# Kernel optimization log

Hardware: AMD Instinct MI355X
Metric: run time of the kernel (lower is better)

## Reference

```python
import jax, jax.numpy as jnp
import numpy as np

WS = 14            # window side (14x14 patches)
DIM = 768          # model dim (ViT-Base)
H = 12             # heads
HD = DIM // H      # head dim = 64
B = 128            # batch
N = WS * WS + 1    # 197 tokens (patches + CLS)
NRD = (2 * WS - 1) ** 2 + 3  # num_relative_distance = 732


def _rel_index():
    # Faithful replication of the torch buffer construction.
    coords = np.stack(np.meshgrid(np.arange(WS), np.arange(WS), indexing='ij'))  # [2,WS,WS]
    flat = coords.reshape(2, -1)                                   # [2, WS*WS]
    rel = flat[:, :, None] - flat[:, None, :]                      # [2, P, P]
    rel = rel.transpose(1, 2, 0).astype(np.int64)                  # [P, P, 2]
    rel[:, :, 0] += WS - 1
    rel[:, :, 1] += WS - 1
    rel[:, :, 0] *= 2 * WS - 1
    idx = np.zeros((N, N), dtype=np.int64)
    idx[1:, 1:] = rel.sum(-1)
    idx[0, :] = NRD - 3
    idx[:, 0] = NRD - 2
    idx[0, 0] = NRD - 1
    return jnp.asarray(idx, dtype=jnp.int32)


def setup_inputs() -> dict:
    key = jax.random.key(0)
    ks = jax.random.split(key, 5)
    return {
        'x': jax.random.normal(ks[0], (B, N, DIM), dtype=jnp.float32),
        'qkv_w': jax.random.normal(ks[1], (3 * DIM, DIM), dtype=jnp.float32) * 0.02,
        'q_bias': jnp.zeros((DIM,), jnp.float32),
        'v_bias': jnp.zeros((DIM,), jnp.float32),
        'rpb_table': jax.random.normal(ks[2], (NRD, H), dtype=jnp.float32) * 0.02,
        'proj_w': jax.random.normal(ks[3], (DIM, DIM), dtype=jnp.float32) * 0.02,
        'proj_b': jnp.zeros((DIM,), jnp.float32),
        'rel_idx': _rel_index(),
    }


def reference(x, qkv_w, q_bias, v_bias, rpb_table, proj_w, proj_b, rel_idx):
    Bv, Nv, C = x.shape
    scale = HD ** -0.5
    # qkv_bias = cat(q_bias, zeros, v_bias); eval mode so dropout is identity
    bias = jnp.concatenate([q_bias, jnp.zeros_like(v_bias), v_bias])
    qkv = x @ qkv_w.T + bias                                   # [B,N,3*DIM]
    qkv = qkv.reshape(Bv, Nv, 3, H, HD).transpose(2, 0, 3, 1, 4)
    q, k, v = qkv[0] * scale, qkv[1], qkv[2]                   # [B,H,N,HD]
    attn = jnp.einsum('bhqd,bhkd->bhqk', q, k)                 # [B,H,N,N]
    rpb = rpb_table[rel_idx]                                   # gather -> [N,N,H]
    attn = attn + rpb.transpose(2, 0, 1)[None]                 # + [1,H,N,N]
    attn = jax.nn.softmax(attn, axis=-1)
    out = jnp.einsum('bhqk,bhkd->bhqd', attn, v)               # [B,H,N,HD]
    out = out.transpose(0, 2, 1, 3).reshape(Bv, Nv, H * HD)
    return out @ proj_w.T + proj_b
```

## Files before the change

kernel.cpp:

```cpp
#include <hip/hip_runtime.h>
#include <hip/hip_bf16.h>
#include <cstdint>

#define BATCH 128
#define NTOK  197
#define NHEAD 12

typedef __attribute__((ext_vector_type(8))) __bf16 bf16x8;
typedef __attribute__((ext_vector_type(4))) float f32x4;
typedef __attribute__((ext_vector_type(4))) unsigned short ushort4v;

#define KSTR 72

__device__ __forceinline__ unsigned short f2bf(float f) {
    union { float f; unsigned int u; } v; v.f = f;
    unsigned int r = (v.u + 0x7FFFu + ((v.u >> 16) & 1u)) >> 16;
    return (unsigned short)r;
}

__device__ __forceinline__ void async_cp16(const void* gsrc, void* lds_dst) {
    __builtin_amdgcn_global_load_lds(
        (const __attribute__((address_space(1))) unsigned int*)((uintptr_t)gsrc),
        (__attribute__((address_space(3))) unsigned int*)((uintptr_t)lds_dst),
        16, 0, 0);
}

__global__ void bias_tiles(const float* __restrict__ rpb,
                           const int* __restrict__ rel_idx,
                           float* __restrict__ BT) {
    int idx = blockIdx.x * 256 + threadIdx.x;
    int r    = idx & 3;
    int j    = (idx >> 2) & 3;
    int l16  = (idx >> 4) & 15;
    int quad = (idx >> 8) & 3;
    int kt   = (idx >> 10) & 3;
    int qt   = (idx >> 12) & 15;
    int h    = idx >> 16;
    int qn = qt * 16 + quad * 4 + r; if (qn > 196) qn = 196;
    int kn = kt * 64 + j * 16 + l16;
    float v = 0.f;
    if (kn < NTOK) v = rpb[rel_idx[qn * NTOK + kn] * NHEAD + h];
    BT[idx] = v;
}

__global__ __launch_bounds__(256) void cvt_bf16(const float4* __restrict__ src,
                                                ushort4v* __restrict__ dst, int n4) {
    int i = blockIdx.x * 256 + threadIdx.x;
    if (i >= n4) return;
    float4 f = src[i];
    ushort4v o;
    o.x = f2bf(f.x); o.y = f2bf(f.y); o.z = f2bf(f.z); o.w = f2bf(f.w);
    dst[i] = o;
}

template <int EPI>
__global__ __launch_bounds__(256) void gemm_mfma(
    const unsigned short* __restrict__ A,
    const unsigned short* __restrict__ W,
    const float* __restrict__ bias1, const float* __restrict__ bias2,
    unsigned short* __restrict__ oq, unsigned short* __restrict__ ok,
    unsigned short* __restrict__ ov, float* __restrict__ outf,
    int Mc) {
    __shared__ unsigned short As[128 * 32];
    __shared__ unsigned short Bs[128 * 32];

    const int t    = threadIdx.x;
    const int lane = t & 63;
    const int wave = t >> 6;
    const int wm   = wave >> 1;
    const int wn   = wave & 1;
    const int quad = lane >> 4;
    const int l16  = lane & 15;
    const int m0   = blockIdx.y * 128;
    const int n0   = blockIdx.x * 128;

    const int srow = lane >> 2;
    const int scol = (lane & 3) * 8;
    int ar0 = m0 + wave * 32 + srow;      if (ar0 >= Mc) ar0 = Mc - 1;
    int ar1 = m0 + wave * 32 + 16 + srow; if (ar1 >= Mc) ar1 = Mc - 1;
    const unsigned short* Ag0 = A + (size_t)ar0 * 768 + scol;
    const unsigned short* Ag1 = A + (size_t)ar1 * 768 + scol;
    const unsigned short* Wg0 = W + (size_t)(n0 + wave * 32 + srow) * 768 + scol;
    const unsigned short* Wg1 = Wg0 + (size_t)16 * 768;
    unsigned short* Ad0 = As + (wave * 32) * 32;
    unsigned short* Ad1 = As + (wave * 32 + 16) * 32;
    unsigned short* Bd0 = Bs + (wave * 32) * 32;
    unsigned short* Bd1 = Bs + (wave * 32 + 16) * 32;

    const unsigned short* Afp = As + (wm * 64 + l16) * 32 + quad * 8;
    const unsigned short* Bfp = Bs + (wn * 64 + l16) * 32 + quad * 8;

    f32x4 acc[4][4] = {};

    for (int k0 = 0; k0 < 768; k0 += 32) {
        __syncthreads();
        async_cp16(Ag0 + k0, Ad0);
        async_cp16(Ag1 + k0, Ad1);
        async_cp16(Wg0 + k0, Bd0);
        async_cp16(Wg1 + k0, Bd1);
        __syncthreads();
        bf16x8 af[4], bfr[4];
#pragma unroll
        for (int i = 0; i < 4; i++) af[i]  = *(const bf16x8*)(Afp + i * 16 * 32);
#pragma unroll
        for (int j = 0; j < 4; j++) bfr[j] = *(const bf16x8*)(Bfp + j * 16 * 32);
#pragma unroll
        for (int i = 0; i < 4; i++)
#pragma unroll
            for (int j = 0; j < 4; j++)
                acc[i][j] = __builtin_amdgcn_mfma_f32_16x16x32_bf16(
                    af[i], bfr[j], acc[i][j], 0, 0, 0);
    }

    if (EPI == 0) {
        const int part   = n0 / 768;
        const float scale = (part == 0) ? 0.125f : 1.f;
        unsigned short* dst = (part == 0) ? oq : (part == 1 ? ok : ov);
        const int nb0 = n0 - part * 768;
#pragma unroll
        for (int j = 0; j < 4; j++) {
            const int nnb = nb0 + wn * 64 + j * 16;
            const int h   = nnb >> 6;
            const int d   = (nnb & 63) + l16;
            const float bb = (part == 0) ? bias1[nnb + l16]
                           : (part == 2 ? bias2[nnb + l16] : 0.f);
#pragma unroll
            for (int i = 0; i < 4; i++) {
                const int mb = m0 + wm * 64 + i * 16 + quad * 4;
#pragma unroll
                for (int r = 0; r < 4; r++) {
                    const int m = mb + r;
                    if (m < Mc) {
                        const int bi  = m / NTOK;
                        const int tok = m - bi * NTOK;
                        dst[(((size_t)bi * NHEAD + h) * NTOK + tok) * 64 + d] =
                            f2bf((acc[i][j][r] + bb) * scale);
                    }
                }
            }
        }
    } else {
#pragma unroll
        for (int j = 0; j < 4; j++) {
            const int col = n0 + wn * 64 + j * 16 + l16;
            const float bb = bias1[col];
#pragma unroll
            for (int i = 0; i < 4; i++) {
                const int mb = m0 + wm * 64 + i * 16 + quad * 4;
#pragma unroll
                for (int r = 0; r < 4; r++) {
                    const int m = mb + r;
                    if (m < Mc) outf[(size_t)m * 768 + col] = acc[i][j][r] + bb;
                }
            }
        }
    }
}

__global__ __launch_bounds__(256, 2) void attn_mfma(
    const unsigned short* __restrict__ Q, const unsigned short* __restrict__ K,
    const unsigned short* __restrict__ V, const float* __restrict__ BT,
    unsigned short* __restrict__ AO) {
    __shared__ unsigned short Ks[64 * KSTR];
    __shared__ unsigned short Vt[64 * KSTR];
    __shared__ unsigned short Ps[4][64 * KSTR];

    const int t    = threadIdx.x;
    const int lane = t & 63;
    const int wave = t >> 6;
    const int quad = lane >> 4;
    const int l16  = lane & 15;
    const int bh   = blockIdx.x;
    const int b    = bh / NHEAD;
    const int h    = bh - b * NHEAD;

    const unsigned short* qb = Q + (size_t)bh * NTOK * 64;
    const unsigned short* kb = K + (size_t)bh * NTOK * 64;
    const unsigned short* vb = V + (size_t)bh * NTOK * 64;

    bf16x8 qf[4][2];
#pragma unroll
    for (int i = 0; i < 4; i++) {
        int tok = wave * 64 + i * 16 + l16; if (tok > 196) tok = 196;
#pragma unroll
        for (int ks = 0; ks < 2; ks++)
            qf[i][ks] = *(const bf16x8*)&qb[(size_t)tok * 64 + ks * 32 + quad * 8];
    }

    f32x4 O[4][4] = {};
    float lsum[4][4] = {};

    for (int kt = 0; kt < 4; kt++) {
        __syncthreads();
        {
            const int row = t >> 2, cg = t & 3;
            int gk = kt * 64 + row; if (gk > 196) gk = 196;
            const uint4* src = (const uint4*)&kb[(size_t)gk * 64 + cg * 16];
            *(uint4*)&Ks[row * KSTR + cg * 16]     = src[0];
            *(uint4*)&Ks[row * KSTR + cg * 16 + 8] = src[1];
        }
        {
            const int key = t & 63, dg = t >> 6;
            int gk = kt * 64 + key; if (gk > 196) gk = 196;
            union { uint4 v4[2]; unsigned short u[16]; } tmp;
            const uint4* src = (const uint4*)&vb[(size_t)gk * 64 + dg * 16];
            tmp.v4[0] = src[0]; tmp.v4[1] = src[1];
#pragma unroll
            for (int u = 0; u < 16; u++) Vt[(dg * 16 + u) * KSTR + key] = tmp.u[u];
        }
        __syncthreads();

        f32x4 acc[4][4];
#pragma unroll
        for (int i = 0; i < 4; i++) {
            const float4* bp = (const float4*)&BT[
                (((((size_t)h * 16 + (wave * 4 + i)) * 4 + kt) * 4 + quad) * 16 + l16) * 16];
#pragma unroll
            for (int j = 0; j < 4; j++) {
                float4 f = bp[j];
                acc[i][j] = (f32x4){f.x, f.y, f.z, f.w};
            }
        }

#pragma unroll
        for (int ks = 0; ks < 2; ks++) {
            bf16x8 kf[4];
#pragma unroll
            for (int j = 0; j < 4; j++)
                kf[j] = *(const bf16x8*)&Ks[(j * 16 + l16) * KSTR + ks * 32 + quad * 8];
#pragma unroll
            for (int i = 0; i < 4; i++)
#pragma unroll
                for (int j = 0; j < 4; j++)
                    acc[i][j] = __builtin_amdgcn_mfma_f32_16x16x32_bf16(
                        qf[i][ks], kf[j], acc[i][j], 0, 0, 0);
        }

#pragma unroll
        for (int j = 0; j < 4; j++) {
            const int kn = kt * 64 + j * 16 + l16;
            const bool kval = (kn < NTOK);
#pragma unroll
            for (int i = 0; i < 4; i++)
#pragma unroll
                for (int r = 0; r < 4; r++) {
                    float p = kval ? __expf(fminf(acc[i][j][r], 30.f)) : 0.f;
                    lsum[i][r] += p;
                    Ps[wave][(i * 16 + quad * 4 + r) * KSTR + j * 16 + l16] = f2bf(p);
                }
        }

#pragma unroll
        for (int ks = 0; ks < 2; ks++) {
            bf16x8 vf[4], pf[4];
#pragma unroll
            for (int jd = 0; jd < 4; jd++)
                vf[jd] = *(const bf16x8*)&Vt[(jd * 16 + l16) * KSTR + ks * 32 + quad * 8];
#pragma unroll
            for (int i = 0; i < 4; i++)
                pf[i] = *(const bf16x8*)&Ps[wave][(i * 16 + l16) * KSTR + ks * 32 + quad * 8];
#pragma unroll
            for (int i = 0; i < 4; i++)
#pragma unroll
                for (int jd = 0; jd < 4; jd++)
                    O[i][jd] = __builtin_amdgcn_mfma_f32_16x16x32_bf16(
                        pf[i], vf[jd], O[i][jd], 0, 0, 0);
        }
    }

#pragma unroll
    for (int i = 0; i < 4; i++)
#pragma unroll
        for (int r = 0; r < 4; r++) {
            float l = lsum[i][r];
            l += __shfl_xor(l, 1); l += __shfl_xor(l, 2);
            l += __shfl_xor(l, 4); l += __shfl_xor(l, 8);
            lsum[i][r] = 1.f / l;
        }
#pragma unroll
    for (int i = 0; i < 4; i++) {
        const int tb = wave * 64 + i * 16 + quad * 4;
#pragma unroll
        for (int r = 0; r < 4; r++) {
            const int tok = tb + r;
            if (tok < NTOK) {
                const float rl = lsum[i][r];
#pragma unroll
                for (int jd = 0; jd < 4; jd++)
                    AO[((size_t)b * NTOK + tok) * 768 + h * 64 + jd * 16 + l16] =
                        f2bf(O[i][jd][r] * rl);
            }
        }
    }
}

extern "C" void kernel_launch(void* const* d_in, const int* in_sizes, int n_in,
                              void* d_out, int out_size, void* d_ws, size_t ws_size,
                              hipStream_t stream) {
    const float* x      = (const float*)d_in[0];
    const float* qkv_w  = (const float*)d_in[1];
    const float* q_bias = (const float*)d_in[2];
    const float* v_bias = (const float*)d_in[3];
    const float* rpb    = (const float*)d_in[4];
    const float* proj_w = (const float*)d_in[5];
    const float* proj_b = (const float*)d_in[6];
    const int*   rel_idx = (const int*)d_in[7];
    float* out = (float*)d_out;

    const size_t EB   = 151296;
    const size_t NBT  = 786432;
    const size_t NX   = (size_t)BATCH * NTOK * 768;
    const size_t NWQ  = (size_t)2304 * 768;
    const size_t NWP  = (size_t)768 * 768;

    const size_t fixed_bytes = NBT * 4 + (NX + NWQ + NWP) * 2;
    int Bc = BATCH;
    while (Bc > 1 && fixed_bytes + 8ull * Bc * EB > ws_size) Bc >>= 1;
    if (fixed_bytes + 8ull * Bc * EB > ws_size) return;
    const int nc = BATCH / Bc;
    const int Mc = Bc * NTOK;
    const int Gy = (Mc + 127) / 128;

    float* BT             = (float*)d_ws;
    unsigned short* xbf   = (unsigned short*)(BT + NBT);
    unsigned short* wqkv  = xbf + NX;
    unsigned short* wproj = wqkv + NWQ;
    unsigned short* q     = wproj + NWP;
    unsigned short* k     = q + (size_t)Bc * EB;
    unsigned short* v     = k + (size_t)Bc * EB;
    unsigned short* aobf  = v + (size_t)Bc * EB;

    bias_tiles<<<(int)(NBT / 256), 256, 0, stream>>>(rpb, rel_idx, BT);
    cvt_bf16<<<(int)((NX / 4 + 255) / 256), 256, 0, stream>>>(
        (const float4*)x, (ushort4v*)xbf, (int)(NX / 4));
    cvt_bf16<<<(int)((NWQ / 4 + 255) / 256), 256, 0, stream>>>(
        (const float4*)qkv_w, (ushort4v*)wqkv, (int)(NWQ / 4));
    cvt_bf16<<<(int)((NWP / 4 + 255) / 256), 256, 0, stream>>>(
        (const float4*)proj_w, (ushort4v*)wproj, (int)(NWP / 4));

    for (int c = 0; c < nc; c++) {
        gemm_mfma<0><<<dim3(2304 / 128, Gy), 256, 0, stream>>>(
            xbf + (size_t)c * Mc * 768, wqkv, q_bias, v_bias, q, k, v, nullptr, Mc);
        attn_mfma<<<Bc * NHEAD, 256, 0, stream>>>(q, k, v, BT, aobf);
        gemm_mfma<1><<<dim3(768 / 128, Gy), 256, 0, stream>>>(
            aobf, wproj, proj_b, nullptr, nullptr, nullptr, nullptr,
            out + (size_t)c * Mc * 768, Mc);
    }
}
```

Before: 472.7 us.

## Write V transposed from QKV GEMM, async-load K/V with swizzled LDS, remap XCD blocks

The QKV GEMM epilogue now writes V pre-transposed, as [b,h,d,256 tokens] zero-padded, so attention can stream K and V^T into LDS with async global-to-LDS copies. This replaces the per-thread scalar transpose scatter and one barrier. LDS tiles in both the GEMM and attention use XOR swizzles instead of padding to avoid bank conflicts. The GEMM also remaps workgroup IDs so neighbouring tiles land on the same XCD, and the MFMA loops raise wave priority. The cost is an extra zero-fill kernel, more workspace, and strided transposed stores in the V epilogue.

```diff
diff --git a/kernel.cpp b/kernel.cpp
--- a/kernel.cpp
+++ b/kernel.cpp
@@ -53,13 +53,19 @@
     dst[i] = o;
 }
 
+__global__ __launch_bounds__(256) void zero_buf(uint4* __restrict__ p, int n) {
+    int i = blockIdx.x * 256 + threadIdx.x;
+    if (i < n) p[i] = (uint4){0u, 0u, 0u, 0u};
+}
+
 template <int EPI>
 __global__ __launch_bounds__(256) void gemm_mfma(
     const unsigned short* __restrict__ A,
     const unsigned short* __restrict__ W,
     const float* __restrict__ bias1, const float* __restrict__ bias2,
     unsigned short* __restrict__ oq, unsigned short* __restrict__ ok,
-    unsigned short* __restrict__ ov, float* __restrict__ outf,
+    unsigned short* __restrict__ ov,
+    float* __restrict__ outf,
     int Mc) {
     __shared__ unsigned short As[128 * 32];
     __shared__ unsigned short Bs[128 * 32];
@@ -71,11 +77,18 @@
     const int wn   = wave & 1;
     const int quad = lane >> 4;
     const int l16  = lane & 15;
-    const int m0   = blockIdx.y * 128;
-    const int n0   = blockIdx.x * 128;
+
+    const int gx  = gridDim.x;
+    const int nwg = gx * gridDim.y;
+    const int orig = blockIdx.y * gx + blockIdx.x;
+    const int q8 = nwg >> 3, r8 = nwg & 7;
+    const int xcd = orig & 7, rest = orig >> 3;
+    const int wg = (xcd < r8 ? xcd * (q8 + 1) : r8 * (q8 + 1) + (xcd - r8) * q8) + rest;
+    const int m0 = (wg / gx) * 128;
+    const int n0 = (wg % gx) * 128;
 
     const int srow = lane >> 2;
-    const int scol = (lane & 3) * 8;
+    const int scol = ((lane & 3) ^ (srow & 3)) * 8;
     int ar0 = m0 + wave * 32 + srow;      if (ar0 >= Mc) ar0 = Mc - 1;
     int ar1 = m0 + wave * 32 + 16 + srow; if (ar1 >= Mc) ar1 = Mc - 1;
     const unsigned short* Ag0 = A + (size_t)ar0 * 768 + scol;
@@ -87,8 +100,8 @@
     unsigned short* Bd0 = Bs + (wave * 32) * 32;
     unsigned short* Bd1 = Bs + (wave * 32 + 16) * 32;
 
-    const unsigned short* Afp = As + (wm * 64 + l16) * 32 + quad * 8;
-    const unsigned short* Bfp = Bs + (wn * 64 + l16) * 32 + quad * 8;
+    const unsigned short* Afp = As + (wm * 64 + l16) * 32 + ((quad ^ (l16 & 3)) * 8);
+    const unsigned short* Bfp = Bs + (wn * 64 + l16) * 32 + ((quad ^ (l16 & 3)) * 8);
 
     f32x4 acc[4][4] = {};
 
@@ -113,28 +126,51 @@
     }
 
     if (EPI == 0) {
-        const int part   = n0 / 768;
-        const float scale = (part == 0) ? 0.125f : 1.f;
-        unsigned short* dst = (part == 0) ? oq : (part == 1 ? ok : ov);
-        const int nb0 = n0 - part * 768;
-#pragma unroll
-        for (int j = 0; j < 4; j++) {
-            const int nnb = nb0 + wn * 64 + j * 16;
-            const int h   = nnb >> 6;
-            const int d   = (nnb & 63) + l16;
-            const float bb = (part == 0) ? bias1[nnb + l16]
-                           : (part == 2 ? bias2[nnb + l16] : 0.f);
-#pragma unroll
-            for (int i = 0; i < 4; i++) {
-                const int mb = m0 + wm * 64 + i * 16 + quad * 4;
-#pragma unroll
-                for (int r = 0; r < 4; r++) {
-                    const int m = mb + r;
-                    if (m < Mc) {
-                        const int bi  = m / NTOK;
-                        const int tok = m - bi * NTOK;
-                        dst[(((size_t)bi * NHEAD + h) * NTOK + tok) * 64 + d] =
-                            f2bf((acc[i][j][r] + bb) * scale);
+        const int part = n0 / 768;
+        const int nb0  = n0 - part * 768;
+        if (part < 2) {
+            const float scale = (part == 0) ? 0.125f : 1.f;
+            unsigned short* dst = (part == 0) ? oq : ok;
+#pragma unroll
+            for (int j = 0; j < 4; j++) {
+                const int nnb = nb0 + wn * 64 + j * 16;
+                const int h   = nnb >> 6;
+                const int d   = (nnb & 63) + l16;
+                const float bb = (part == 0) ? bias1[nnb + l16] : 0.f;
+#pragma unroll
+                for (int i = 0; i < 4; i++) {
+                    const int mb = m0 + wm * 64 + i * 16 + quad * 4;
+#pragma unroll
+                    for (int r = 0; r < 4; r++) {
+                        const int m = mb + r;
+                        if (m < Mc) {
+                            const int bi  = m / NTOK;
+                            const int tok = m - bi * NTOK;
+                            dst[(((size_t)bi * NHEAD + h) * NTOK + tok) * 64 + d] =
+                                f2bf((acc[i][j][r] + bb) * scale);
+                        }
+                    }
+                }
+            }
+        } else {
+#pragma unroll
+            for (int j = 0; j < 4; j++) {
+                const int nnb = nb0 + wn * 64 + j * 16;
+                const int h   = nnb >> 6;
+                const int d   = (nnb & 63) + l16;
+                const float bb = bias2[nnb + l16];
+#pragma unroll
+                for (int i = 0; i < 4; i++) {
+                    const int mb = m0 + wm * 64 + i * 16 + quad * 4;
+#pragma unroll
+                    for (int r = 0; r < 4; r++) {
+                        const int m = mb + r;
+                        if (m < Mc) {
+                            const int bi  = m / NTOK;
+                            const int tok = m - bi * NTOK;
+                            ov[(((size_t)bi * NHEAD + h) * 64 + d) * 256 + tok] =
+                                f2bf(acc[i][j][r] + bb);
+                        }
                     }
                 }
             }
@@ -159,10 +195,10 @@
 
 __global__ __launch_bounds__(256, 2) void attn_mfma(
     const unsigned short* __restrict__ Q, const unsigned short* __restrict__ K,
-    const unsigned short* __restrict__ V, const float* __restrict__ BT,
+    const unsigned short* __restrict__ VT, const float* __restrict__ BT,
     unsigned short* __restrict__ AO) {
-    __shared__ unsigned short Ks[64 * KSTR];
-    __shared__ unsigned short Vt[64 * KSTR];
+    __shared__ unsigned short Ks[64 * 64];
+    __shared__ unsigned short Vt[64 * 64];
     __shared__ unsigned short Ps[4][64 * KSTR];
 
     const int t    = threadIdx.x;
@@ -174,9 +210,9 @@
     const int b    = bh / NHEAD;
     const int h    = bh - b * NHEAD;
 
-    const unsigned short* qb = Q + (size_t)bh * NTOK * 64;
-    const unsigned short* kb = K + (size_t)bh * NTOK * 64;
-    const unsigned short* vb = V + (size_t)bh * NTOK * 64;
+    const unsigned short* qb  = Q  + (size_t)bh * NTOK * 64;
+    const unsigned short* kb  = K  + (size_t)bh * NTOK * 64;
+    const unsigned short* vtg = VT + (size_t)bh * 64 * 256;
 
     bf16x8 qf[4][2];
 #pragma unroll
@@ -193,22 +229,16 @@
     for (int kt = 0; kt < 4; kt++) {
         __syncthreads();
         {
-            const int row = t >> 2, cg = t & 3;
-            int gk = kt * 64 + row; if (gk > 196) gk = 196;
-            const uint4* src = (const uint4*)&kb[(size_t)gk * 64 + cg * 16];
-            *(uint4*)&Ks[row * KSTR + cg * 16]     = src[0];
-            *(uint4*)&Ks[row * KSTR + cg * 16 + 8] = src[1];
-        }
-        {
-            const int key = t & 63, dg = t >> 6;
-            int gk = kt * 64 + key; if (gk > 196) gk = 196;
-            union { uint4 v4[2]; unsigned short u[16]; } tmp;
-            const uint4* src = (const uint4*)&vb[(size_t)gk * 64 + dg * 16];
-            tmp.v4[0] = src[0]; tmp.v4[1] = src[1];
-#pragma unroll
-            for (int u = 0; u < 16; u++) Vt[(dg * 16 + u) * KSTR + key] = tmp.u[u];
-        }
-        __syncthreads();
+            const int rsub = wave * 8 + (lane >> 3);
+            const int chk  = ((lane & 7) ^ (lane >> 3)) * 8;
+            int gk0 = kt * 64 + rsub;      if (gk0 > 196) gk0 = 196;
+            int gk1 = kt * 64 + 32 + rsub; if (gk1 > 196) gk1 = 196;
+            async_cp16(kb + (size_t)gk0 * 64 + chk, Ks + wave * 512);
+            async_cp16(kb + (size_t)gk1 * 64 + chk, Ks + 2048 + wave * 512);
+            async_cp16(vtg + (size_t)rsub * 256 + kt * 64 + chk, Vt + wave * 512);
+            async_cp16(vtg + (size_t)(32 + rsub) * 256 + kt * 64 + chk,
+                       Vt + 2048 + wave * 512);
+        }
 
         f32x4 acc[4][4];
 #pragma unroll
@@ -222,18 +252,24 @@
             }
         }
 
+        asm volatile("s_waitcnt vmcnt(0)" ::: "memory");
+        __builtin_amdgcn_s_barrier();
+
 #pragma unroll
         for (int ks = 0; ks < 2; ks++) {
             bf16x8 kf[4];
 #pragma unroll
             for (int j = 0; j < 4; j++)
-                kf[j] = *(const bf16x8*)&Ks[(j * 16 + l16) * KSTR + ks * 32 + quad * 8];
+                kf[j] = *(const bf16x8*)&Ks[(j * 16 + l16) * 64 +
+                                            (((ks * 4 + quad) ^ (l16 & 7)) * 8)];
+            __builtin_amdgcn_s_setprio(1);
 #pragma unroll
             for (int i = 0; i < 4; i++)
 #pragma unroll
                 for (int j = 0; j < 4; j++)
                     acc[i][j] = __builtin_amdgcn_mfma_f32_16x16x32_bf16(
                         qf[i][ks], kf[j], acc[i][j], 0, 0, 0);
+            __builtin_amdgcn_s_setprio(0);
         }
 
 #pragma unroll
@@ -255,16 +291,19 @@
             bf16x8 vf[4], pf[4];
 #pragma unroll
             for (int jd = 0; jd < 4; jd++)
-                vf[jd] = *(const bf16x8*)&Vt[(jd * 16 + l16) * KSTR + ks * 32 + quad * 8];
+                vf[jd] = *(const bf16x8*)&Vt[(jd * 16 + l16) * 64 +
+                                             (((ks * 4 + quad) ^ (l16 & 7)) * 8)];
 #pragma unroll
             for (int i = 0; i < 4; i++)
                 pf[i] = *(const bf16x8*)&Ps[wave][(i * 16 + l16) * KSTR + ks * 32 + quad * 8];
+            __builtin_amdgcn_s_setprio(1);
 #pragma unroll
             for (int i = 0; i < 4; i++)
 #pragma unroll
                 for (int jd = 0; jd < 4; jd++)
                     O[i][jd] = __builtin_amdgcn_mfma_f32_16x16x32_bf16(
                         pf[i], vf[jd], O[i][jd], 0, 0, 0);
+            __builtin_amdgcn_s_setprio(0);
         }
     }
 
@@ -308,15 +347,17 @@
     float* out = (float*)d_out;
 
     const size_t EB   = 151296;
+    const size_t VTE  = 196608;
     const size_t NBT  = 786432;
     const size_t NX   = (size_t)BATCH * NTOK * 768;
     const size_t NWQ  = (size_t)2304 * 768;
     const size_t NWP  = (size_t)768 * 768;
 
     const size_t fixed_bytes = NBT * 4 + (NX + NWQ + NWP) * 2;
+    const size_t per_b = 2ull * (3 * EB + VTE);
     int Bc = BATCH;
-    while (Bc > 1 && fixed_bytes + 8ull * Bc * EB > ws_size) Bc >>= 1;
-    if (fixed_bytes + 8ull * Bc * EB > ws_size) return;
+    while (Bc > 1 && fixed_bytes + (size_t)Bc * per_b > ws_size) Bc >>= 1;
+    if (fixed_bytes + (size_t)Bc * per_b > ws_size) return;
     const int nc = BATCH / Bc;
     const int Mc = Bc * NTOK;
     const int Gy = (Mc + 127) / 128;
@@ -327,9 +368,11 @@
     unsigned short* wproj = wqkv + NWQ;
     unsigned short* q     = wproj + NWP;
     unsigned short* k     = q + (size_t)Bc * EB;
-    unsigned short* v     = k + (size_t)Bc * EB;
-    unsigned short* aobf  = v + (size_t)Bc * EB;
-
+    unsigned short* vt    = k + (size_t)Bc * EB;
+    unsigned short* aobf  = vt + (size_t)Bc * VTE;
+
+    const int nz = Bc * 24576;
+    zero_buf<<<(nz + 255) / 256, 256, 0, stream>>>((uint4*)vt, nz);
     bias_tiles<<<(int)(NBT / 256), 256, 0, stream>>>(rpb, rel_idx, BT);
     cvt_bf16<<<(int)((NX / 4 + 255) / 256), 256, 0, stream>>>(
         (const float4*)x, (ushort4v*)xbf, (int)(NX / 4));
@@ -340,8 +383,8 @@
 
     for (int c = 0; c < nc; c++) {
         gemm_mfma<0><<<dim3(2304 / 128, Gy), 256, 0, stream>>>(
-            xbf + (size_t)c * Mc * 768, wqkv, q_bias, v_bias, q, k, v, nullptr, Mc);
-        attn_mfma<<<Bc * NHEAD, 256, 0, stream>>>(q, k, v, BT, aobf);
+            xbf + (size_t)c * Mc * 768, wqkv, q_bias, v_bias, q, k, vt, nullptr, Mc);
+        attn_mfma<<<Bc * NHEAD, 256, 0, stream>>>(q, k, vt, BT, aobf);
         gemm_mfma<1><<<dim3(768 / 128, Gy), 256, 0, stream>>>(
             aobf, wproj, proj_b, nullptr, nullptr, nullptr, nullptr,
             out + (size_t)c * Mc * 768, Mc);
```

Measured after the change: 460.3 us. -2.6%, faster.
